# Kernel tuning notes

Measured on AMD Instinct MI355X. Metric: run time of the kernel, lower is better.

The kernel has to match this reference:

```python
import jax, jax.numpy as jnp
import numpy as np

NEG = -1000000.0  # same finite mask value as the Triton kernel


def setup_inputs() -> dict:
    key = jax.random.key(0)
    k1, k2, k3, k4 = jax.random.split(key, 4)
    B, H, KVH, S, D = 1, 32, 8, 2048, 128
    return {
        "q": jax.random.normal(k1, (B, H, S, D), dtype=jnp.float32),
        "k": jax.random.normal(k2, (B, KVH, S, D), dtype=jnp.float32),
        "v": jax.random.normal(k3, (B, KVH, S, D), dtype=jnp.float32),
        "sinks": jax.random.normal(k4, (H,), dtype=jnp.float32),
        "bandwidth": 1024,
    }


def reference(q, k, v, sinks, bandwidth):
    """Prefill flash attention with causal + sliding-window masking, GQA, and
    per-head attention sinks (extra logit in the softmax denominator)."""
    B, H, S, D = q.shape
    ratio = H // k.shape[1]  # KV_HEAD_RATIO
    kf = jnp.repeat(k, ratio, axis=1)  # [B,H,S,D]
    vf = jnp.repeat(v, ratio, axis=1)
    sm_scale = 1.0 / np.sqrt(D).astype(np.float32)

    logits = jnp.einsum("bhqd,bhkd->bhqk", q, kf) * sm_scale  # [B,H,S,S]
    q_pos = jnp.arange(S)[:, None]
    k_pos = jnp.arange(S)[None, :]
    mask = k_pos > q_pos  # causal
    if bandwidth > 0:
        mask = mask | (k_pos < q_pos - bandwidth + 1)  # sliding window
    logits = jnp.where(mask, NEG, logits)

    sink = sinks[None, :, None]  # [1,H,1] broadcast over batch, query
    m = jnp.maximum(jnp.max(logits, axis=-1), sink)  # [B,H,S]
    p = jnp.exp(logits - m[..., None])
    denom = p.sum(axis=-1) + jnp.exp(sink - m)  # sink contributes to denom only
    out = jnp.einsum("bhqk,bhkd->bhqd", p, vf) / denom[..., None]
    return out
```

## Files before the change

kernel.cpp:

```cpp
#include <hip/hip_runtime.h>
#include <hip/hip_bf16.h>

typedef __bf16 bf16x8 __attribute__((ext_vector_type(8)));
typedef unsigned short u16x8 __attribute__((ext_vector_type(8)));
typedef unsigned int u32x4 __attribute__((ext_vector_type(4)));
typedef float f32x4 __attribute__((ext_vector_type(4)));

#define SLEN 2048
#define DDIM 128
#define NH   32
#define NKVH 8
#define KVB  32
#define MINIT  -1e30f
#define MASKED -3e30f

static __device__ __forceinline__ unsigned short f2bfu(float f) {
  union { float f; unsigned u; } x; x.f = f;
  return (unsigned short)((x.u + 0x7fffu + ((x.u >> 16) & 1u)) >> 16);
}
static __device__ __forceinline__ float bfu2f(unsigned short u) {
  union { unsigned u; float f; } x; x.u = ((unsigned)u) << 16;
  return x.f;
}
static __device__ __forceinline__ unsigned cvt_pk_bf16(float lo, float hi) {
  unsigned r;
  asm("v_cvt_pk_bf16_f32 %0, %1, %2" : "=v"(r) : "v"(lo), "v"(hi));
  return r;
}
static __device__ __forceinline__ f32x4 mfma_bf16(u16x8 a, u16x8 b, f32x4 c) {
  return __builtin_amdgcn_mfma_f32_16x16x32_bf16(
      __builtin_bit_cast(bf16x8, a), __builtin_bit_cast(bf16x8, b), c, 0, 0, 0);
}
static __device__ __forceinline__ void gload16(const unsigned short* g, unsigned short* l) {
  __builtin_amdgcn_global_load_lds(
      (const __attribute__((address_space(1))) unsigned*)g,
      (__attribute__((address_space(3))) unsigned*)l, 16, 0, 0);
}

__global__ __launch_bounds__(256) void conv_kv(const float* __restrict__ k,
                                               const float* __restrict__ v,
                                               unsigned* __restrict__ kdst,
                                               unsigned short* __restrict__ vt) {
  __shared__ unsigned T32[32][17];
  const int bb = blockIdx.x;
  if (bb < 1024) {
    const int i = bb * 256 + threadIdx.x;
    const float4 f0 = ((const float4*)k)[2 * i];
    const float4 f1 = ((const float4*)k)[2 * i + 1];
    u32x4 o = { cvt_pk_bf16(f0.x, f0.y), cvt_pk_bf16(f0.z, f0.w),
                cvt_pk_bf16(f1.x, f1.y), cvt_pk_bf16(f1.z, f1.w) };
    ((u32x4*)kdst)[i] = o;
    return;
  }
  const int b   = bb - 1024;
  const int dt  = b & 3;
  const int st  = (b >> 2) & 63;
  const int kvh = b >> 8;
  const int r  = threadIdx.x >> 3;
  const int cg = threadIdx.x & 7;
  const float4 f = *(const float4*)(v + ((size_t)(kvh * SLEN + st * 32 + r) * DDIM) + dt * 32 + cg * 4);
  T32[r][cg * 2]     = cvt_pk_bf16(f.x, f.y);
  T32[r][cg * 2 + 1] = cvt_pk_bf16(f.z, f.w);
  __syncthreads();
  const int dr = threadIdx.x >> 3;
  const unsigned sel = (dr & 1) ? 0x07060302u : 0x05040100u;
  const unsigned a0 = T32[cg * 4 + 0][dr >> 1], a1 = T32[cg * 4 + 1][dr >> 1];
  const unsigned a2 = T32[cg * 4 + 2][dr >> 1], a3 = T32[cg * 4 + 3][dr >> 1];
  unsigned short* vp = vt + (size_t)kvh * DDIM * SLEN + (size_t)(dt * 32 + dr) * SLEN + st * 32 + cg * 4;
  const unsigned w0 = __builtin_amdgcn_perm(a1, a0, sel);
  const unsigned w1 = __builtin_amdgcn_perm(a3, a2, sel);
  vp[0] = (unsigned short)(w0 & 0xffff);
  vp[1] = (unsigned short)(w0 >> 16);
  vp[2] = (unsigned short)(w1 & 0xffff);
  vp[3] = (unsigned short)(w1 >> 16);
}

template <int NCH>
__global__ __launch_bounds__(256, 4) void attn_fwd(
    const float* __restrict__ q, const unsigned short* __restrict__ kbf,
    const unsigned short* __restrict__ vtg, const float* __restrict__ sinks,
    const int* __restrict__ bwp, float* __restrict__ out,
    unsigned short* __restrict__ pO, float* __restrict__ pm,
    float* __restrict__ pl) {
  constexpr int NQT = 32;
  __shared__ unsigned short KB[2][KVB][DDIM];
  __shared__ unsigned short VB[2][DDIM][KVB];
  __shared__ unsigned Pex[4][16][16];
  __shared__ float SmS[4][16];

  const int tid  = threadIdx.x;
  const int wid  = tid >> 6;
  const int lane = tid & 63;
  const int ln   = lane & 15;
  const int hi   = lane >> 4;

  const int B   = blockIdx.x;
  const int x   = B & 7;
  const int j   = B >> 3;
  constexpr int per = 4 * NCH;
  const int qt  = NQT - 1 - (j / per);
  const int rem = j % per;
  const int hh  = rem / NCH;
  const int c   = rem % NCH;
  const int h   = x * 4 + hh;
  const int kvh = x;
  const int q0  = qt * 64;
  const int qrow0 = q0 + wid * 16;
  const int qpos  = qrow0 + ln;

  const int bwv    = bwp[0];
  const int lo_off = (bwv > 0) ? (bwv - 1) : SLEN;

  const int T0 = max(0, q0 - lo_off) >> 5;
  const int T1 = (q0 + 63) >> 5;
  const int N  = T1 - T0 + 1;
  const int ch = (N + NCH - 1) / NCH;
  const int Ts = T0 + c * ch;
  const int Te = min(T1, Ts + ch - 1);

  const float sm_scale = 0.08838834764831845f;

  u16x8 qf[4];
  {
    const float* qp = q + ((size_t)(h * SLEN + qpos) * DDIM) + hi * 8;
    #pragma unroll
    for (int dk = 0; dk < 4; ++dk) {
      float4 f0 = *(const float4*)(qp + dk * 32);
      float4 f1 = *(const float4*)(qp + dk * 32 + 4);
      u32x4 t = { cvt_pk_bf16(f0.x, f0.y), cvt_pk_bf16(f0.z, f0.w),
                  cvt_pk_bf16(f1.x, f1.y), cvt_pk_bf16(f1.z, f1.w) };
      qf[dk] = __builtin_bit_cast(u16x8, t);
    }
  }

  float m_ln = MINIT, l_ln = 0.0f;
  f32x4 oacc[8];
  #pragma unroll
  for (int nt = 0; nt < 8; ++nt) oacc[nt] = f32x4{0.f, 0.f, 0.f, 0.f};

  const unsigned short* Kg = kbf + (size_t)kvh * SLEN * DDIM;
  const unsigned short* Vg = vtg + (size_t)kvh * DDIM * SLEN;

  int koff[2], voff[2];
  #pragma unroll
  for (int c2 = 0; c2 < 2; ++c2) {
    const int r = wid * 8 + c2 * 4 + (lane >> 4);
    koff[c2] = r * DDIM + (((lane & 15) ^ (r & 7)) * 8);
    const int d = wid * 32 + c2 * 16 + (lane >> 2);
    voff[c2] = d * SLEN + (((lane & 3) ^ ((lane >> 3) & 3)) * 8);
  }

  int kfo[4];
  #pragma unroll
  for (int dk = 0; dk < 4; ++dk)
    kfo[dk] = ln * DDIM + (((dk * 4 + hi) ^ (ln & 7)) * 8);
  const int vswz = (hi ^ ((ln >> 1) & 3)) * 8;

  if (Ts <= Te) {
    const int kbS = Ts * 32, kbE = Te * 32;

    {
      gload16(Kg + (size_t)kbS * DDIM + koff[0], &KB[0][wid * 8][0]);
      gload16(Kg + (size_t)kbS * DDIM + koff[1], &KB[0][wid * 8 + 4][0]);
      gload16(Vg + (size_t)kbS + voff[0], &VB[0][wid * 32][0]);
      gload16(Vg + (size_t)kbS + voff[1], &VB[0][wid * 32 + 16][0]);
    }

    int cur = 0;
    for (int kb = kbS; kb <= kbE; kb += KVB) {
      __syncthreads();

      if (kb + KVB <= kbE) {
        const int nb = kb + KVB;
        const int nxt = cur ^ 1;
        gload16(Kg + (size_t)nb * DDIM + koff[0], &KB[nxt][wid * 8][0]);
        gload16(Kg + (size_t)nb * DDIM + koff[1], &KB[nxt][wid * 8 + 4][0]);
        gload16(Vg + (size_t)nb + voff[0], &VB[nxt][wid * 32][0]);
        gload16(Vg + (size_t)nb + voff[1], &VB[nxt][wid * 32 + 16][0]);
      }

      const bool skip = (kb > qrow0 + 15) || (kb + KVB - 1 < qrow0 - lo_off);
      if (!skip) {
        const unsigned short* kbp = &KB[cur][0][0];
        const unsigned short* vbp = &VB[cur][0][0];

        f32x4 sacc0 = {0,0,0,0}, sacc1 = {0,0,0,0};
        #pragma unroll
        for (int dk = 0; dk < 4; ++dk) {
          sacc0 = mfma_bf16(*(const u16x8*)(kbp + kfo[dk]), qf[dk], sacc0);
          sacc1 = mfma_bf16(*(const u16x8*)(kbp + kfo[dk] + 16 * DDIM), qf[dk], sacc1);
        }

        float p[8];
        #pragma unroll
        for (int r = 0; r < 4; ++r) {
          const int kp0 = kb + hi * 4 + r;
          const int kp1 = kp0 + 16;
          p[r]     = ((kp0 <= qpos) && (kp0 >= qpos - lo_off)) ? sacc0[r] * sm_scale : MASKED;
          p[4 + r] = ((kp1 <= qpos) && (kp1 >= qpos - lo_off)) ? sacc1[r] * sm_scale : MASKED;
        }

        float mx = fmaxf(fmaxf(fmaxf(p[0], p[1]), fmaxf(p[2], p[3])),
                         fmaxf(fmaxf(p[4], p[5]), fmaxf(p[6], p[7])));
        mx = fmaxf(mx, __shfl_xor(mx, 16));
        mx = fmaxf(mx, __shfl_xor(mx, 32));

        if (__any(mx > m_ln + 8.0f)) {
          const float mn   = fmaxf(m_ln, mx);
          const float corr = __expf(m_ln - mn);
          l_ln *= corr;
          m_ln = mn;
          if (hi == 0) SmS[wid][ln] = corr;
          float c4[4];
          #pragma unroll
          for (int r = 0; r < 4; ++r) c4[r] = SmS[wid][hi * 4 + r];
          #pragma unroll
          for (int nt = 0; nt < 8; ++nt)
            #pragma unroll
            for (int r = 0; r < 4; ++r) oacc[nt][r] *= c4[r];
        }

        float s = 0.0f;
        #pragma unroll
        for (int jj = 0; jj < 8; ++jj) { p[jj] = __expf(p[jj] - m_ln); s += p[jj]; }
        s += __shfl_xor(s, 16);
        s += __shfl_xor(s, 32);
        l_ln += s;

        Pex[wid][ln][hi * 2]         = cvt_pk_bf16(p[0], p[1]);
        Pex[wid][ln][hi * 2 + 1]     = cvt_pk_bf16(p[2], p[3]);
        Pex[wid][ln][8 + hi * 2]     = cvt_pk_bf16(p[4], p[5]);
        Pex[wid][ln][8 + hi * 2 + 1] = cvt_pk_bf16(p[6], p[7]);
        const u16x8 pa = __builtin_bit_cast(u16x8, *(const u32x4*)&Pex[wid][ln][hi * 4]);

        #pragma unroll
        for (int nt = 0; nt < 8; ++nt) {
          const u16x8 vb = *(const u16x8*)(vbp + (nt * 16 + ln) * KVB + vswz);
          oacc[nt] = mfma_bf16(pa, vb, oacc[nt]);
        }
      }
      cur ^= 1;
    }
  }

  if (NCH == 1) {
    const float sink = sinks[h];
    const float M  = fmaxf(m_ln, sink);
    const float ed = __expf(m_ln - M);
    const float fac_ln = ed / (l_ln * ed + __expf(sink - M));
    if (hi == 0) SmS[wid][ln] = fac_ln;
    float fac4[4];
    #pragma unroll
    for (int r = 0; r < 4; ++r) fac4[r] = SmS[wid][hi * 4 + r];
    #pragma unroll
    for (int r = 0; r < 4; ++r) {
      float* op = out + ((size_t)(h * SLEN + qrow0 + hi*4 + r) * DDIM) + ln;
      #pragma unroll
      for (int nt = 0; nt < 8; ++nt) op[nt * 16] = oacc[nt][r] * fac4[r];
    }
  } else {
    const size_t Lb = ((size_t)(h * NQT + qt)) * NCH + c;
    if (hi == 0) {
      pm[Lb * 64 + wid * 16 + ln] = m_ln;
      pl[Lb * 64 + wid * 16 + ln] = l_ln;
    }
    #pragma unroll
    for (int r = 0; r < 4; ++r) {
      unsigned short* po = pO + (Lb * 64 + wid * 16 + hi * 4 + r) * 128 + ln;
      #pragma unroll
      for (int nt = 0; nt < 8; ++nt) po[nt * 16] = f2bfu(oacc[nt][r]);
    }
  }
}

template <int NCH, int QBLK, int NQT>
__global__ __launch_bounds__(256) void mergeN(
    const unsigned short* __restrict__ pO, const float* __restrict__ pm,
    const float* __restrict__ pl, const float* __restrict__ sinks,
    float* __restrict__ out) {
  const int t    = blockIdx.x * 256 + threadIdx.x;
  const int rid  = t >> 2;
  const int d0   = (t & 3) * 32;
  const int h    = rid >> 11;
  const int qpos = rid & 2047;
  const int qt   = qpos / QBLK;
  const int lr   = qpos % QBLK;
  const size_t base = ((size_t)(h * NQT + qt) * NCH) * QBLK + lr;
  const float sink = sinks[h];
  float mc[NCH], lc[NCH];
  float M = sink;
  #pragma unroll
  for (int c = 0; c < NCH; ++c) {
    mc[c] = pm[base + (size_t)c * QBLK];
    lc[c] = pl[base + (size_t)c * QBLK];
    M = fmaxf(M, mc[c]);
  }
  float denom = __expf(sink - M);
  float sc[NCH];
  #pragma unroll
  for (int c = 0; c < NCH; ++c) { sc[c] = __expf(mc[c] - M); denom += lc[c] * sc[c]; }
  const float inv = 1.0f / denom;
  float o[32];
  #pragma unroll
  for (int i = 0; i < 32; ++i) o[i] = 0.f;
  #pragma unroll
  for (int c = 0; c < NCH; ++c) {
    const unsigned short* pp = pO + (base + (size_t)c * QBLK) * 128 + d0;
    const float s = sc[c] * inv;
    #pragma unroll
    for (int i = 0; i < 4; ++i) {
      u16x8 a = *(const u16x8*)(pp + i * 8);
      #pragma unroll
      for (int jj = 0; jj < 8; ++jj) o[i*8+jj] += bfu2f(a[jj]) * s;
    }
  }
  float* op = out + (size_t)rid * 128 + d0;
  #pragma unroll
  for (int i = 0; i < 8; ++i)
    *(float4*)(op + i*4) = make_float4(o[i*4], o[i*4+1], o[i*4+2], o[i*4+3]);
}

extern "C" void kernel_launch(void* const* d_in, const int* in_sizes, int n_in,
                              void* d_out, int out_size, void* d_ws, size_t ws_size,
                              hipStream_t stream) {
  const float* q     = (const float*)d_in[0];
  const float* k     = (const float*)d_in[1];
  const float* v     = (const float*)d_in[2];
  const float* sinks = (const float*)d_in[3];
  const int*   bw    = (const int*)d_in[4];
  float* out = (float*)d_out;

  const size_t kvElems = (size_t)NKVH * SLEN * DDIM;
  unsigned short* kbf = (unsigned short*)d_ws;
  unsigned short* vtg = kbf + kvElems;
  unsigned short* pO  = vtg + kvElems;

  const size_t nPart2 = (size_t)NH * 32 * 2 * 64;
  const size_t need2  = 4 * kvElems + nPart2 * 128 * 2 + nPart2 * 8;

  conv_kv<<<dim3(1024 + NKVH * 64 * 4), 256, 0, stream>>>(k, v, (unsigned*)kbf, vtg);

  if (ws_size >= need2) {
    float* pm = (float*)(pO + nPart2 * 128);
    float* pl = pm + nPart2;
    attn_fwd<2><<<dim3(2048), 256, 0, stream>>>(q, kbf, vtg, sinks, bw, out, pO, pm, pl);
    mergeN<2, 64, 32><<<dim3(1024), 256, 0, stream>>>(pO, pm, pl, sinks, out);
  } else {
    attn_fwd<1><<<dim3(1024), 256, 0, stream>>>(q, kbf, vtg, sinks, bw, out, pO, nullptr, nullptr);
  }
}
```

Before: 85.83 us.

## Stage KV tiles through registers and permute K rows to drop P LDS exchange

Replaces the double-buffered direct global-to-LDS loads with register prefetch of the next K/V tile, followed by a synchronous store into a single LDS buffer each iteration. It also permutes which K rows each lane's QK MFMA covers, so each lane's P values already sit in the layout the PV MFMA operand needs. This removes the Pex shared-memory round trip. The cost is a second __syncthreads per iteration, half the LDS buffering, and extra register pressure from the prefetched vectors.

```diff
diff --git a/kernel.cpp b/kernel.cpp
--- a/kernel.cpp
+++ b/kernel.cpp
@@ -31,10 +31,8 @@
   return __builtin_amdgcn_mfma_f32_16x16x32_bf16(
       __builtin_bit_cast(bf16x8, a), __builtin_bit_cast(bf16x8, b), c, 0, 0, 0);
 }
-static __device__ __forceinline__ void gload16(const unsigned short* g, unsigned short* l) {
-  __builtin_amdgcn_global_load_lds(
-      (const __attribute__((address_space(1))) unsigned*)g,
-      (__attribute__((address_space(3))) unsigned*)l, 16, 0, 0);
+static __device__ __forceinline__ int vswz_k(int row) {
+  return (row & 3) | (((row >> 3) & 1) << 2);
 }
 
 __global__ __launch_bounds__(256) void conv_kv(const float* __restrict__ k,
@@ -83,9 +81,8 @@
     unsigned short* __restrict__ pO, float* __restrict__ pm,
     float* __restrict__ pl) {
   constexpr int NQT = 32;
-  __shared__ unsigned short KB[2][KVB][DDIM];
-  __shared__ unsigned short VB[2][DDIM][KVB];
-  __shared__ unsigned Pex[4][16][16];
+  __shared__ unsigned short Kl[KVB * DDIM];
+  __shared__ unsigned short Vt[DDIM * KVB];
   __shared__ float SmS[4][16];
 
   const int tid  = threadIdx.x;
@@ -141,105 +138,107 @@
   const unsigned short* Kg = kbf + (size_t)kvh * SLEN * DDIM;
   const unsigned short* Vg = vtg + (size_t)kvh * DDIM * SLEN;
 
-  int koff[2], voff[2];
-  #pragma unroll
-  for (int c2 = 0; c2 < 2; ++c2) {
-    const int r = wid * 8 + c2 * 4 + (lane >> 4);
-    koff[c2] = r * DDIM + (((lane & 15) ^ (r & 7)) * 8);
-    const int d = wid * 32 + c2 * 16 + (lane >> 2);
-    voff[c2] = d * SLEN + (((lane & 3) ^ ((lane >> 3) & 3)) * 8);
-  }
-
+  const int kr0 = tid >> 4, sk = tid & 15;
+  const int kr1 = kr0 + 16;
+  const int kw0 = kr0 * DDIM + (((sk & 8) | ((sk & 7) ^ vswz_k(kr0))) * 8);
+  const int kw1 = kr1 * DDIM + (((sk & 8) | ((sk & 7) ^ vswz_k(kr1))) * 8);
+  const int vr0 = tid >> 2, sv = tid & 3;
+  const int vr1 = vr0 + 64;
+  const int vw0 = vr0 * KVB + ((sv ^ ((vr0 >> 1) & 3)) * 8);
+  const int vw1 = vr1 * KVB + ((sv ^ ((vr1 >> 1) & 3)) * 8);
+
+  const int prow = ((ln >> 2) << 3) | (ln & 3);
+  const int vk   = (ln & 3) | (((ln >> 2) & 1) << 2);
   int kfo[4];
   #pragma unroll
-  for (int dk = 0; dk < 4; ++dk)
-    kfo[dk] = ln * DDIM + (((dk * 4 + hi) ^ (ln & 7)) * 8);
-  const int vswz = (hi ^ ((ln >> 1) & 3)) * 8;
+  for (int dk = 0; dk < 4; ++dk) {
+    const int s = dk * 4 + hi;
+    kfo[dk] = prow * DDIM + (((s & 8) | ((s & 7) ^ vk)) * 8);
+  }
+  const int vro = ln * KVB + ((hi ^ ((ln >> 1) & 3)) * 8);
 
   if (Ts <= Te) {
     const int kbS = Ts * 32, kbE = Te * 32;
 
+    u16x8 pk0, pk1, pv0, pv1;
     {
-      gload16(Kg + (size_t)kbS * DDIM + koff[0], &KB[0][wid * 8][0]);
-      gload16(Kg + (size_t)kbS * DDIM + koff[1], &KB[0][wid * 8 + 4][0]);
-      gload16(Vg + (size_t)kbS + voff[0], &VB[0][wid * 32][0]);
-      gload16(Vg + (size_t)kbS + voff[1], &VB[0][wid * 32 + 16][0]);
-    }
-
-    int cur = 0;
+      pk0 = *(const u16x8*)(Kg + (size_t)(kbS + kr0) * DDIM + sk * 8);
+      pk1 = *(const u16x8*)(Kg + (size_t)(kbS + kr1) * DDIM + sk * 8);
+      pv0 = *(const u16x8*)(Vg + (size_t)vr0 * SLEN + kbS + sv * 8);
+      pv1 = *(const u16x8*)(Vg + (size_t)vr1 * SLEN + kbS + sv * 8);
+    }
+
     for (int kb = kbS; kb <= kbE; kb += KVB) {
       __syncthreads();
-
-      if (kb + KVB <= kbE) {
-        const int nb = kb + KVB;
-        const int nxt = cur ^ 1;
-        gload16(Kg + (size_t)nb * DDIM + koff[0], &KB[nxt][wid * 8][0]);
-        gload16(Kg + (size_t)nb * DDIM + koff[1], &KB[nxt][wid * 8 + 4][0]);
-        gload16(Vg + (size_t)nb + voff[0], &VB[nxt][wid * 32][0]);
-        gload16(Vg + (size_t)nb + voff[1], &VB[nxt][wid * 32 + 16][0]);
-      }
-
-      const bool skip = (kb > qrow0 + 15) || (kb + KVB - 1 < qrow0 - lo_off);
-      if (!skip) {
-        const unsigned short* kbp = &KB[cur][0][0];
-        const unsigned short* vbp = &VB[cur][0][0];
-
-        f32x4 sacc0 = {0,0,0,0}, sacc1 = {0,0,0,0};
+      *(u16x8*)&Kl[kw0] = pk0;
+      *(u16x8*)&Kl[kw1] = pk1;
+      *(u16x8*)&Vt[vw0] = pv0;
+      *(u16x8*)&Vt[vw1] = pv1;
+      __syncthreads();
+
+      {
+        const int nb = min(kb + KVB, kbE);
+        pk0 = *(const u16x8*)(Kg + (size_t)(nb + kr0) * DDIM + sk * 8);
+        pk1 = *(const u16x8*)(Kg + (size_t)(nb + kr1) * DDIM + sk * 8);
+        pv0 = *(const u16x8*)(Vg + (size_t)vr0 * SLEN + nb + sv * 8);
+        pv1 = *(const u16x8*)(Vg + (size_t)vr1 * SLEN + nb + sv * 8);
+      }
+
+      if (kb > qrow0 + 15) continue;
+      if (kb + KVB - 1 < qrow0 - lo_off) continue;
+
+      f32x4 sacc0 = {0,0,0,0}, sacc1 = {0,0,0,0};
+      #pragma unroll
+      for (int dk = 0; dk < 4; ++dk) {
+        sacc0 = mfma_bf16(*(const u16x8*)&Kl[kfo[dk]], qf[dk], sacc0);
+        sacc1 = mfma_bf16(*(const u16x8*)&Kl[kfo[dk] + 4 * DDIM], qf[dk], sacc1);
+      }
+
+      float p[8];
+      #pragma unroll
+      for (int r = 0; r < 4; ++r) {
+        const int kp0 = kb + hi * 8 + r;
+        const int kp1 = kp0 + 4;
+        p[r]     = ((kp0 <= qpos) && (kp0 >= qpos - lo_off)) ? sacc0[r] * sm_scale : MASKED;
+        p[4 + r] = ((kp1 <= qpos) && (kp1 >= qpos - lo_off)) ? sacc1[r] * sm_scale : MASKED;
+      }
+
+      float mx = fmaxf(fmaxf(fmaxf(p[0], p[1]), fmaxf(p[2], p[3])),
+                       fmaxf(fmaxf(p[4], p[5]), fmaxf(p[6], p[7])));
+      mx = fmaxf(mx, __shfl_xor(mx, 16));
+      mx = fmaxf(mx, __shfl_xor(mx, 32));
+
+      if (__any(mx > m_ln + 8.0f)) {
+        const float mn   = fmaxf(m_ln, mx);
+        const float corr = __expf(m_ln - mn);
+        l_ln *= corr;
+        m_ln = mn;
+        if (hi == 0) SmS[wid][ln] = corr;
+        float c4[4];
         #pragma unroll
-        for (int dk = 0; dk < 4; ++dk) {
-          sacc0 = mfma_bf16(*(const u16x8*)(kbp + kfo[dk]), qf[dk], sacc0);
-          sacc1 = mfma_bf16(*(const u16x8*)(kbp + kfo[dk] + 16 * DDIM), qf[dk], sacc1);
-        }
-
-        float p[8];
+        for (int r = 0; r < 4; ++r) c4[r] = SmS[wid][hi * 4 + r];
         #pragma unroll
-        for (int r = 0; r < 4; ++r) {
-          const int kp0 = kb + hi * 4 + r;
-          const int kp1 = kp0 + 16;
-          p[r]     = ((kp0 <= qpos) && (kp0 >= qpos - lo_off)) ? sacc0[r] * sm_scale : MASKED;
-          p[4 + r] = ((kp1 <= qpos) && (kp1 >= qpos - lo_off)) ? sacc1[r] * sm_scale : MASKED;
-        }
-
-        float mx = fmaxf(fmaxf(fmaxf(p[0], p[1]), fmaxf(p[2], p[3])),
-                         fmaxf(fmaxf(p[4], p[5]), fmaxf(p[6], p[7])));
-        mx = fmaxf(mx, __shfl_xor(mx, 16));
-        mx = fmaxf(mx, __shfl_xor(mx, 32));
-
-        if (__any(mx > m_ln + 8.0f)) {
-          const float mn   = fmaxf(m_ln, mx);
-          const float corr = __expf(m_ln - mn);
-          l_ln *= corr;
-          m_ln = mn;
-          if (hi == 0) SmS[wid][ln] = corr;
-          float c4[4];
+        for (int nt = 0; nt < 8; ++nt)
           #pragma unroll
-          for (int r = 0; r < 4; ++r) c4[r] = SmS[wid][hi * 4 + r];
-          #pragma unroll
-          for (int nt = 0; nt < 8; ++nt)
-            #pragma unroll
-            for (int r = 0; r < 4; ++r) oacc[nt][r] *= c4[r];
-        }
-
-        float s = 0.0f;
-        #pragma unroll
-        for (int jj = 0; jj < 8; ++jj) { p[jj] = __expf(p[jj] - m_ln); s += p[jj]; }
-        s += __shfl_xor(s, 16);
-        s += __shfl_xor(s, 32);
-        l_ln += s;
-
-        Pex[wid][ln][hi * 2]         = cvt_pk_bf16(p[0], p[1]);
-        Pex[wid][ln][hi * 2 + 1]     = cvt_pk_bf16(p[2], p[3]);
-        Pex[wid][ln][8 + hi * 2]     = cvt_pk_bf16(p[4], p[5]);
-        Pex[wid][ln][8 + hi * 2 + 1] = cvt_pk_bf16(p[6], p[7]);
-        const u16x8 pa = __builtin_bit_cast(u16x8, *(const u32x4*)&Pex[wid][ln][hi * 4]);
-
-        #pragma unroll
-        for (int nt = 0; nt < 8; ++nt) {
-          const u16x8 vb = *(const u16x8*)(vbp + (nt * 16 + ln) * KVB + vswz);
-          oacc[nt] = mfma_bf16(pa, vb, oacc[nt]);
-        }
-      }
-      cur ^= 1;
+          for (int r = 0; r < 4; ++r) oacc[nt][r] *= c4[r];
+      }
+
+      float s = 0.0f;
+      #pragma unroll
+      for (int jj = 0; jj < 8; ++jj) { p[jj] = __expf(p[jj] - m_ln); s += p[jj]; }
+      s += __shfl_xor(s, 16);
+      s += __shfl_xor(s, 32);
+      l_ln += s;
+
+      const u32x4 paw = { cvt_pk_bf16(p[0], p[1]), cvt_pk_bf16(p[2], p[3]),
+                          cvt_pk_bf16(p[4], p[5]), cvt_pk_bf16(p[6], p[7]) };
+      const u16x8 pa = __builtin_bit_cast(u16x8, paw);
+
+      #pragma unroll
+      for (int nt = 0; nt < 8; ++nt) {
+        const u16x8 vb = *(const u16x8*)&Vt[vro + nt * 16 * KVB];
+        oacc[nt] = mfma_bf16(pa, vb, oacc[nt]);
+      }
     }
   }
 
```

Measured after the change: 75.27 us. 12.3% less time.
